# Performance work log

Hardware: AMD Instinct MI355X
Metric: run time of the kernel (lower is better)

Reference implementation:

```python
import jax, jax.numpy as jnp
import numpy as np

N = 63001
F_IN = 512
F_OUT = 256
E = 2_000_000
LRELU_ALPHA = 0.2


def setup_inputs() -> dict:
    key = jax.random.key(0)
    ks = jax.random.split(key, 10)
    x = jax.random.normal(ks[0], (N, F_IN), dtype=jnp.float32)
    values = jax.random.uniform(ks[1], (E,), dtype=jnp.float32)
    edge_index = jax.random.randint(ks[2], (2, E), 0, N, dtype=jnp.int32)
    # learned params: conv1d kernel_size=1 == dense matmuls
    W = jax.random.normal(ks[3], (F_IN, F_OUT), dtype=jnp.float32) * (1.0 / np.sqrt(F_IN))
    a1 = jax.random.normal(ks[4], (F_OUT,), dtype=jnp.float32) * (1.0 / np.sqrt(F_OUT))
    b1 = jnp.zeros((), dtype=jnp.float32)
    a2 = jax.random.normal(ks[5], (F_OUT,), dtype=jnp.float32) * (1.0 / np.sqrt(F_OUT))
    b2 = jnp.zeros((), dtype=jnp.float32)
    b_out = jnp.zeros((F_OUT,), dtype=jnp.float32)
    return {"x": x, "values": values, "edge_index": edge_index,
            "W": W, "a1": a1, "b1": b1, "a2": a2, "b2": b2, "b_out": b_out}


def reference(x, values, edge_index, W, a1, b1, a2, b2, b_out):
    src = edge_index[0]  # row index i of sparse adjacency entry
    dst = edge_index[1]  # col index j

    # conv1d(kernel=1) projections == matmuls
    seq_fts = x @ W                      # [N, F_out]
    f1 = seq_fts @ a1 + b1               # [N]
    f2 = seq_fts @ a2 + b2               # [N]

    # edgewise logits: s_ij * f1_i + s_ij * f2_j  (sparse_add of two masked broadcasts)
    logits = values * (f1[src] + f2[dst])           # [E]
    logits = jax.nn.leaky_relu(logits, LRELU_ALPHA)

    # sparse row-wise softmax over edges grouped by src
    m = jax.ops.segment_max(logits, src, num_segments=N)   # [N]
    p = jnp.exp(logits - m[src])                            # [E]
    denom = jax.ops.segment_sum(p, src, num_segments=N)     # [N]
    coefs = p / denom[src]                                  # [E]

    # SPMM: out_i = sum_j coef_ij * seq_fts_j
    out = jnp.zeros((N, F_OUT), dtype=seq_fts.dtype)
    out = out.at[src].add(coefs[:, None] * seq_fts[dst])

    out = out + b_out                                       # bias_add
    return jax.nn.elu(out)
```

## Files before the change

kernel.cpp:

```cpp
#include <hip/hip_runtime.h>
#include <cstdint>
#include <cstddef>

#define FIN 512
#define FOUT 256
#define LRELU 0.2f
#define NBKT 8
#define BSH 13

typedef __attribute__((ext_vector_type(8))) short bf16x8;
typedef __attribute__((ext_vector_type(8))) unsigned short u16x8;
typedef __attribute__((ext_vector_type(4))) float f32x4;
typedef _Float16 h16x2 __attribute__((ext_vector_type(2)));

#define PERM_LO 0x05040100u
#define PERM_HI 0x07060302u
#define ONE2H   0x3C003C00u

__device__ inline ushort f2bf(float f) {
    union { float f; uint32_t u; } c; c.f = f;
    uint32_t u = c.u;
    return (ushort)((u + 0x7FFF + ((u >> 16) & 1)) >> 16);
}
__device__ inline ushort f2h(float f) {
    union { _Float16 h; ushort u; } c; c.h = (_Float16)f;
    return c.u;
}
__device__ inline h16x2 u2h2(uint32_t u) {
    union { uint32_t u; h16x2 h; } c; c.u = u;
    return c.h;
}

__global__ void prep_wt(const float* __restrict__ W, ushort* __restrict__ WT)
{
    const int idx = blockIdx.x * blockDim.x + threadIdx.x;
    if (idx < FIN * FOUT) {
        const int k = idx >> 8, n = idx & 255;
        WT[(size_t)n * FIN + k] = f2bf(W[(size_t)k * FOUT + n]);
    }
}

#define BM 128
#define BK 64
__global__ __launch_bounds__(512) void gemm_bf16(
    const float* __restrict__ A,
    const ushort* __restrict__ BT,
    ushort* __restrict__ Ch,
    const float* __restrict__ a1, const float* __restrict__ a2,
    const float* __restrict__ b1, const float* __restrict__ b2,
    float* __restrict__ f1, float* __restrict__ f2,
    int M)
{
    __shared__ ushort As[BM * BK];
    __shared__ ushort Bs[FOUT * BK];
    __shared__ float f1s[BM][2];
    __shared__ float f2s[BM][2];
    const int t = threadIdx.x;
    const int lane = t & 63, w = t >> 6;
    const int wm = w & 3, wn = w >> 2;
    const int brow = blockIdx.x * BM;

    f32x4 acc[2][8] = {};

    const int ar = t >> 2;
    const int ak = (t & 3) << 4;
    const int bcol = t >> 1;
    const int bkc = (t & 1) * 4;

    for (int k0 = 0; k0 < FIN; k0 += BK) {
        {
            f32x4 v0, v1, v2, v3;
            const int grow = brow + ar;
            if (grow < M) {
                const f32x4* p = (const f32x4*)(A + (size_t)grow * FIN + k0 + ak);
                v0 = __builtin_nontemporal_load(p + 0);
                v1 = __builtin_nontemporal_load(p + 1);
                v2 = __builtin_nontemporal_load(p + 2);
                v3 = __builtin_nontemporal_load(p + 3);
            } else {
                v0 = v1 = v2 = v3 = (f32x4)0.f;
            }
            u16x8 w0, w1;
            w0[0]=f2bf(v0[0]); w0[1]=f2bf(v0[1]); w0[2]=f2bf(v0[2]); w0[3]=f2bf(v0[3]);
            w0[4]=f2bf(v1[0]); w0[5]=f2bf(v1[1]); w0[6]=f2bf(v1[2]); w0[7]=f2bf(v1[3]);
            w1[0]=f2bf(v2[0]); w1[1]=f2bf(v2[1]); w1[2]=f2bf(v2[2]); w1[3]=f2bf(v2[3]);
            w1[4]=f2bf(v3[0]); w1[5]=f2bf(v3[1]); w1[6]=f2bf(v3[2]); w1[7]=f2bf(v3[3]);
            const int c0 = ((ak >> 3) + 0) ^ (ar & 7);
            const int c1 = ((ak >> 3) + 1) ^ (ar & 7);
            *(u16x8*)(&As[ar * BK + (c0 << 3)]) = w0;
            *(u16x8*)(&As[ar * BK + (c1 << 3)]) = w1;
        }
        {
            const ushort* bp = BT + (size_t)bcol * FIN + k0;
#pragma unroll
            for (int j = 0; j < 4; ++j) {
                const int c = bkc + j;
                u16x8 bv = *(const u16x8*)(bp + (c << 3));
                *(u16x8*)(&Bs[bcol * BK + ((c ^ (bcol & 7)) << 3)]) = bv;
            }
        }
        __syncthreads();

#pragma unroll
        for (int kk = 0; kk < 2; ++kk) {
            const int kc = kk * 4 + (lane >> 4);
            bf16x8 af[2], bfr[8];
#pragma unroll
            for (int m = 0; m < 2; ++m) {
                const int row = wm * 32 + m * 16 + (lane & 15);
                af[m] = *(const bf16x8*)(&As[row * BK + ((kc ^ (row & 7)) << 3)]);
            }
#pragma unroll
            for (int n = 0; n < 8; ++n) {
                const int col = wn * 128 + n * 16 + (lane & 15);
                bfr[n] = *(const bf16x8*)(&Bs[col * BK + ((kc ^ (col & 7)) << 3)]);
            }
#pragma unroll
            for (int m = 0; m < 2; ++m)
#pragma unroll
                for (int n = 0; n < 8; ++n)
                    acc[m][n] = __builtin_amdgcn_mfma_f32_16x16x32_bf16(
                        af[m], bfr[n], acc[m][n], 0, 0, 0);
        }
        __syncthreads();
    }

    float a1c[8], a2c[8];
#pragma unroll
    for (int n = 0; n < 8; ++n) {
        const int col = wn * 128 + n * 16 + (lane & 15);
        a1c[n] = a1[col];
        a2c[n] = a2[col];
    }
    const int cbase = wn * 128 + (lane & 15);
#pragma unroll
    for (int m = 0; m < 2; ++m) {
#pragma unroll
        for (int reg = 0; reg < 4; ++reg) {
            const int rloc = wm * 32 + m * 16 + (lane >> 4) * 4 + reg;
            const int r = brow + rloc;
            float p1 = 0.f, p2 = 0.f;
#pragma unroll
            for (int n = 0; n < 8; ++n) {
                p1 += acc[m][n][reg] * a1c[n];
                p2 += acc[m][n][reg] * a2c[n];
            }
#pragma unroll
            for (int off = 1; off < 16; off <<= 1) {
                p1 += __shfl_xor(p1, off);
                p2 += __shfl_xor(p2, off);
            }
            if ((lane & 15) == 0) {
                f1s[rloc][wn] = p1;
                f2s[rloc][wn] = p2;
            }
            if (r < M) {
#pragma unroll
                for (int n = 0; n < 8; ++n)
                    Ch[(size_t)r * FOUT + cbase + n * 16] = f2h(acc[m][n][reg]);
            }
        }
    }
    __syncthreads();
    if (t < BM) {
        const int r = brow + t;
        if (r < M) {
            f1[r] = f1s[t][0] + f1s[t][1] + b1[0];
            f2[r] = f2s[t][0] + f2s[t][1] + b2[0];
        }
    }
}

__global__ void pos_kernel(const int* __restrict__ src, const int* __restrict__ dst,
                           int* __restrict__ cnt, int* __restrict__ pos, int E)
{
    int i = (blockIdx.x * blockDim.x + threadIdx.x) * 4;
    if (i + 4 <= E) {
        const int4 s = *(const int4*)(src + i);
        const int4 d = *(const int4*)(dst + i);
        int4 p;
        p.x = atomicAdd(&cnt[s.x * NBKT + (d.x >> BSH)], 1);
        p.y = atomicAdd(&cnt[s.y * NBKT + (d.y >> BSH)], 1);
        p.z = atomicAdd(&cnt[s.z * NBKT + (d.z >> BSH)], 1);
        p.w = atomicAdd(&cnt[s.w * NBKT + (d.w >> BSH)], 1);
        *(int4*)(pos + i) = p;
    } else {
        for (; i < E; ++i) pos[i] = atomicAdd(&cnt[src[i] * NBKT + (dst[i] >> BSH)], 1);
    }
}

__global__ __launch_bounds__(1024) void scan_blk(const int* __restrict__ cnt,
                                                 int* __restrict__ btot, int K)
{
    __shared__ int s[1024];
    const int t = threadIdx.x;
    const int idx = blockIdx.x * 1024 + t;
    s[t] = (idx < K) ? cnt[idx] : 0;
    __syncthreads();
    for (int off = 512; off; off >>= 1) {
        if (t < off) s[t] += s[t + off];
        __syncthreads();
    }
    if (t == 0) btot[blockIdx.x] = s[0];
}

__global__ __launch_bounds__(1024) void scan_top(const int* __restrict__ btot,
                                                 int* __restrict__ boff, int nb)
{
    __shared__ int s[1024];
    const int t = threadIdx.x;
    const int mine = (t < nb) ? btot[t] : 0;
    s[t] = mine;
    __syncthreads();
    for (int off = 1; off < 1024; off <<= 1) {
        const int u = (t >= off) ? s[t - off] : 0;
        __syncthreads();
        s[t] += u;
        __syncthreads();
    }
    if (t < nb) boff[t] = s[t] - mine;
}

__global__ __launch_bounds__(1024) void scan_out(const int* __restrict__ cnt,
                                                 const int* __restrict__ boff,
                                                 int* __restrict__ koff, int K)
{
    __shared__ int s[1024];
    const int t = threadIdx.x;
    const int b = blockIdx.x;
    const int idx = b * 1024 + t;
    const int v = (idx < K) ? cnt[idx] : 0;
    s[t] = v;
    __syncthreads();
    for (int off = 1; off < 1024; off <<= 1) {
        const int u = (t >= off) ? s[t - off] : 0;
        __syncthreads();
        s[t] += u;
        __syncthreads();
    }
    if (idx < K)      koff[idx] = boff[b] + s[t] - v;
    if (idx == K - 1) koff[K]   = boff[b] + s[t];
}

__global__ void scatter_p(const int* __restrict__ src, const int* __restrict__ dst,
                          const float* __restrict__ values, const int* __restrict__ pos,
                          const float* __restrict__ f1, const float* __restrict__ f2,
                          const int* __restrict__ koff,
                          unsigned long long* __restrict__ pd, int E)
{
    const int i = blockIdx.x * blockDim.x + threadIdx.x;
    if (i < E) {
        const int s = src[i];
        const int d = dst[i];
        float lg = values[i] * (f1[s] + f2[d]);
        lg = (lg > 0.f) ? lg : LRELU * lg;
        const float p = __expf(lg);
        const unsigned long long rec = (unsigned long long)f2h(p) |
                                       ((unsigned long long)(uint32_t)d << 32);
        __builtin_nontemporal_store(rec, &pd[koff[s * NBKT + (d >> BSH)] + pos[i]]);
    }
}

__global__ __launch_bounds__(256) void spmm_kernel(
    const ushort* __restrict__ seq,
    const unsigned long long* __restrict__ pd,
    const int* __restrict__ koff, const float* __restrict__ b_out,
    float* __restrict__ out, int N)
{
    const int w = threadIdx.x >> 6, lane = threadIdx.x & 63;
    const int row = blockIdx.x * 4 + w;
    if (row >= N) return;
    const int start = __builtin_amdgcn_readfirstlane(koff[row * NBKT]);
    const int end   = __builtin_amdgcn_readfirstlane(koff[(row + 1) * NBKT]);

    const ushort* seql = seq + lane * 4;
    float acc0 = 0.f, acc1 = 0.f, acc2 = 0.f, acc3 = 0.f, den = 0.f;
    const h16x2 one2 = u2h2(ONE2H);

    int t = start;
    for (; t + 4 <= end; t += 4) {
        const unsigned long long q0 = pd[t],     q1 = pd[t + 1];
        const unsigned long long q2 = pd[t + 2], q3 = pd[t + 3];
        const int d0 = (int)(q0 >> 32), d1 = (int)(q1 >> 32);
        const int d2 = (int)(q2 >> 32), d3 = (int)(q3 >> 32);
        const uint2 s0 = *(const uint2*)(seql + (size_t)d0 * FOUT);
        const uint2 s1 = *(const uint2*)(seql + (size_t)d1 * FOUT);
        const uint2 s2 = *(const uint2*)(seql + (size_t)d2 * FOUT);
        const uint2 s3 = *(const uint2*)(seql + (size_t)d3 * FOUT);
        const h16x2 ppA = u2h2(((uint32_t)q0 & 0xffffu) | ((uint32_t)q1 << 16));
        const h16x2 ppB = u2h2(((uint32_t)q2 & 0xffffu) | ((uint32_t)q3 << 16));
        acc0 = __builtin_amdgcn_fdot2(ppA, u2h2(__builtin_amdgcn_perm(s1.x, s0.x, PERM_LO)), acc0, false);
        acc1 = __builtin_amdgcn_fdot2(ppA, u2h2(__builtin_amdgcn_perm(s1.x, s0.x, PERM_HI)), acc1, false);
        acc2 = __builtin_amdgcn_fdot2(ppA, u2h2(__builtin_amdgcn_perm(s1.y, s0.y, PERM_LO)), acc2, false);
        acc3 = __builtin_amdgcn_fdot2(ppA, u2h2(__builtin_amdgcn_perm(s1.y, s0.y, PERM_HI)), acc3, false);
        den  = __builtin_amdgcn_fdot2(ppA, one2, den, false);
        acc0 = __builtin_amdgcn_fdot2(ppB, u2h2(__builtin_amdgcn_perm(s3.x, s2.x, PERM_LO)), acc0, false);
        acc1 = __builtin_amdgcn_fdot2(ppB, u2h2(__builtin_amdgcn_perm(s3.x, s2.x, PERM_HI)), acc1, false);
        acc2 = __builtin_amdgcn_fdot2(ppB, u2h2(__builtin_amdgcn_perm(s3.y, s2.y, PERM_LO)), acc2, false);
        acc3 = __builtin_amdgcn_fdot2(ppB, u2h2(__builtin_amdgcn_perm(s3.y, s2.y, PERM_HI)), acc3, false);
        den  = __builtin_amdgcn_fdot2(ppB, one2, den, false);
    }
    if (t + 2 <= end) {
        const unsigned long long q0 = pd[t], q1 = pd[t + 1];
        const int d0 = (int)(q0 >> 32), d1 = (int)(q1 >> 32);
        const uint2 s0 = *(const uint2*)(seql + (size_t)d0 * FOUT);
        const uint2 s1 = *(const uint2*)(seql + (size_t)d1 * FOUT);
        const h16x2 ppA = u2h2(((uint32_t)q0 & 0xffffu) | ((uint32_t)q1 << 16));
        acc0 = __builtin_amdgcn_fdot2(ppA, u2h2(__builtin_amdgcn_perm(s1.x, s0.x, PERM_LO)), acc0, false);
        acc1 = __builtin_amdgcn_fdot2(ppA, u2h2(__builtin_amdgcn_perm(s1.x, s0.x, PERM_HI)), acc1, false);
        acc2 = __builtin_amdgcn_fdot2(ppA, u2h2(__builtin_amdgcn_perm(s1.y, s0.y, PERM_LO)), acc2, false);
        acc3 = __builtin_amdgcn_fdot2(ppA, u2h2(__builtin_amdgcn_perm(s1.y, s0.y, PERM_HI)), acc3, false);
        den  = __builtin_amdgcn_fdot2(ppA, one2, den, false);
        t += 2;
    }
    if (t < end) {
        const unsigned long long q0 = pd[t];
        const int d0 = (int)(q0 >> 32);
        const uint2 s0 = *(const uint2*)(seql + (size_t)d0 * FOUT);
        const h16x2 ppA = u2h2((uint32_t)q0 & 0xffffu);
        acc0 = __builtin_amdgcn_fdot2(ppA, u2h2(__builtin_amdgcn_perm(s0.x, s0.x, PERM_LO)), acc0, false);
        acc1 = __builtin_amdgcn_fdot2(ppA, u2h2(__builtin_amdgcn_perm(s0.x, s0.x, PERM_HI)), acc1, false);
        acc2 = __builtin_amdgcn_fdot2(ppA, u2h2(__builtin_amdgcn_perm(s0.y, s0.y, PERM_LO)), acc2, false);
        acc3 = __builtin_amdgcn_fdot2(ppA, u2h2(__builtin_amdgcn_perm(s0.y, s0.y, PERM_HI)), acc3, false);
        den  = __builtin_amdgcn_fdot2(ppA, one2, den, false);
    }

    const float inv = (end > start) ? 1.f / den : 0.f;
    const float4 bo = *(const float4*)(b_out + lane * 4);
    f32x4 o;
    o[0] = acc0 * inv + bo.x;
    o[1] = acc1 * inv + bo.y;
    o[2] = acc2 * inv + bo.z;
    o[3] = acc3 * inv + bo.w;
    o[0] = (o[0] > 0.f) ? o[0] : expm1f(o[0]);
    o[1] = (o[1] > 0.f) ? o[1] : expm1f(o[1]);
    o[2] = (o[2] > 0.f) ? o[2] : expm1f(o[2]);
    o[3] = (o[3] > 0.f) ? o[3] : expm1f(o[3]);
    __builtin_nontemporal_store(o, (f32x4*)(out + (size_t)row * FOUT + lane * 4));
}

extern "C" void kernel_launch(void* const* d_in, const int* in_sizes, int n_in,
                              void* d_out, int out_size, void* d_ws, size_t ws_size,
                              hipStream_t stream)
{
    const float* x      = (const float*)d_in[0];
    const float* values = (const float*)d_in[1];
    const int*   ei     = (const int*)d_in[2];
    const float* W      = (const float*)d_in[3];
    const float* a1     = (const float*)d_in[4];
    const float* b1     = (const float*)d_in[5];
    const float* a2     = (const float*)d_in[6];
    const float* b2     = (const float*)d_in[7];
    const float* b_out  = (const float*)d_in[8];
    float* out = (float*)d_out;

    const int N = in_sizes[0] / FIN;
    const int E = in_sizes[1];
    const int* src = ei;
    const int* dst = ei + E;
    const int K = N * NBKT;

    auto alignup = [](size_t v) { return (v + 255) & ~(size_t)255; };
    char* ws = (char*)d_ws;
    size_t off = 0;
    ushort* seqh  = (ushort*)(ws + off); off = alignup(off + (size_t)N * FOUT * 2);
    ushort* WT    = (ushort*)(ws + off); off = alignup(off + (size_t)FIN * FOUT * 2);
    float*  f1    = (float*)(ws + off);  off = alignup(off + (size_t)N * 4);
    float*  f2    = (float*)(ws + off);  off = alignup(off + (size_t)N * 4);
    int*    cnt   = (int*)(ws + off);    off = alignup(off + (size_t)K * 4);
    int*    koff  = (int*)(ws + off);    off = alignup(off + (size_t)(K + 1) * 4);
    int*    btot  = (int*)(ws + off);    off = alignup(off + (size_t)1024 * 4);
    int*    boff  = (int*)(ws + off);    off = alignup(off + (size_t)1024 * 4);
    int*    pos   = (int*)(ws + off);    off = alignup(off + (size_t)E * 4);
    unsigned long long* pd = (unsigned long long*)(ws + off); off = alignup(off + (size_t)E * 8);
    (void)ws_size;

    const int nbk = (K + 1023) / 1024;

    hipMemsetAsync(cnt, 0, (size_t)K * 4, stream);

    pos_kernel<<<(E / 4 + 255) / 256, 256, 0, stream>>>(src, dst, cnt, pos, E);
    scan_blk<<<nbk, 1024, 0, stream>>>(cnt, btot, K);
    scan_top<<<1, 1024, 0, stream>>>(btot, boff, nbk);
    scan_out<<<nbk, 1024, 0, stream>>>(cnt, boff, koff, K);

    prep_wt<<<(FIN * FOUT + 255) / 256, 256, 0, stream>>>(W, WT);
    gemm_bf16<<<(N + BM - 1) / BM, 512, 0, stream>>>(x, WT, seqh, a1, a2, b1, b2,
                                                     f1, f2, N);

    scatter_p<<<(E + 255) / 256, 256, 0, stream>>>(src, dst, values, pos, f1, f2,
                                                   koff, pd, E);

    spmm_kernel<<<(N + 3) / 4, 256, 0, stream>>>(seqh, pd, koff, b_out, out, N);
}
```

Baseline: 357.5 us.

## Pack edge records to 32 bits, use cursor atomics, and DMA GEMM B tiles into LDS

```diff
diff --git a/kernel.cpp b/kernel.cpp
--- a/kernel.cpp
+++ b/kernel.cpp
@@ -1,4 +1,5 @@
 #include <hip/hip_runtime.h>
+#include <hip/hip_bf16.h>
 #include <cstdint>
 #include <cstddef>
 
@@ -18,9 +19,9 @@
 #define ONE2H   0x3C003C00u
 
 __device__ inline ushort f2bf(float f) {
-    union { float f; uint32_t u; } c; c.f = f;
-    uint32_t u = c.u;
-    return (ushort)((u + 0x7FFF + ((u >> 16) & 1)) >> 16);
+    __hip_bfloat16 h = __float2bfloat16(f);
+    union { __hip_bfloat16 h; ushort u; } c; c.h = h;
+    return c.u;
 }
 __device__ inline ushort f2h(float f) {
     union { _Float16 h; ushort u; } c; c.h = (_Float16)f;
@@ -29,6 +30,9 @@
 __device__ inline h16x2 u2h2(uint32_t u) {
     union { uint32_t u; h16x2 h; } c; c.u = u;
     return c.h;
+}
+__device__ inline float hdot2(h16x2 pp, uint32_t sv, float acc) {
+    return __builtin_amdgcn_fdot2(pp, u2h2(sv), acc, false);
 }
 
 __global__ void prep_wt(const float* __restrict__ W, ushort* __restrict__ WT)
@@ -64,10 +68,22 @@
 
     const int ar = t >> 2;
     const int ak = (t & 3) << 4;
-    const int bcol = t >> 1;
-    const int bkc = (t & 1) * 4;
+
+    const int bcol8 = (lane >> 3);
+    const int bslot = lane & 7;
+    const int bcdat = bslot ^ (bcol8 & 7);
 
     for (int k0 = 0; k0 < FIN; k0 += BK) {
+#pragma unroll
+        for (int j = 0; j < 4; ++j) {
+            const int grp = w * 4 + j;
+            const int col = grp * 8 + bcol8;
+            const ushort* gsrc = BT + (size_t)col * FIN + k0 + bcdat * 8;
+            ushort* ldst = &Bs[grp * 512];
+            __builtin_amdgcn_global_load_lds(
+                (const __attribute__((address_space(1))) void*)gsrc,
+                (__attribute__((address_space(3))) void*)ldst, 16, 0, 0);
+        }
         {
             f32x4 v0, v1, v2, v3;
             const int grow = brow + ar;
@@ -90,15 +106,6 @@
             *(u16x8*)(&As[ar * BK + (c0 << 3)]) = w0;
             *(u16x8*)(&As[ar * BK + (c1 << 3)]) = w1;
         }
-        {
-            const ushort* bp = BT + (size_t)bcol * FIN + k0;
-#pragma unroll
-            for (int j = 0; j < 4; ++j) {
-                const int c = bkc + j;
-                u16x8 bv = *(const u16x8*)(bp + (c << 3));
-                *(u16x8*)(&Bs[bcol * BK + ((c ^ (bcol & 7)) << 3)]) = bv;
-            }
-        }
         __syncthreads();
 
 #pragma unroll
@@ -171,21 +178,19 @@
     }
 }
 
-__global__ void pos_kernel(const int* __restrict__ src, const int* __restrict__ dst,
-                           int* __restrict__ cnt, int* __restrict__ pos, int E)
+__global__ void cnt_kernel(const int* __restrict__ src, const int* __restrict__ dst,
+                           int* __restrict__ cnt, int E)
 {
     int i = (blockIdx.x * blockDim.x + threadIdx.x) * 4;
     if (i + 4 <= E) {
         const int4 s = *(const int4*)(src + i);
         const int4 d = *(const int4*)(dst + i);
-        int4 p;
-        p.x = atomicAdd(&cnt[s.x * NBKT + (d.x >> BSH)], 1);
-        p.y = atomicAdd(&cnt[s.y * NBKT + (d.y >> BSH)], 1);
-        p.z = atomicAdd(&cnt[s.z * NBKT + (d.z >> BSH)], 1);
-        p.w = atomicAdd(&cnt[s.w * NBKT + (d.w >> BSH)], 1);
-        *(int4*)(pos + i) = p;
+        atomicAdd(&cnt[s.x * NBKT + (d.x >> BSH)], 1);
+        atomicAdd(&cnt[s.y * NBKT + (d.y >> BSH)], 1);
+        atomicAdd(&cnt[s.z * NBKT + (d.z >> BSH)], 1);
+        atomicAdd(&cnt[s.w * NBKT + (d.w >> BSH)], 1);
     } else {
-        for (; i < E; ++i) pos[i] = atomicAdd(&cnt[src[i] * NBKT + (dst[i] >> BSH)], 1);
+        for (; i < E; ++i) atomicAdd(&cnt[src[i] * NBKT + (dst[i] >> BSH)], 1);
     }
 }
 
@@ -223,7 +228,8 @@
 
 __global__ __launch_bounds__(1024) void scan_out(const int* __restrict__ cnt,
                                                  const int* __restrict__ boff,
-                                                 int* __restrict__ koff, int K)
+                                                 int* __restrict__ koff,
+                                                 int* __restrict__ cursor, int K)
 {
     __shared__ int s[1024];
     const int t = threadIdx.x;
@@ -238,15 +244,19 @@
         s[t] += u;
         __syncthreads();
     }
-    if (idx < K)      koff[idx] = boff[b] + s[t] - v;
-    if (idx == K - 1) koff[K]   = boff[b] + s[t];
+    if (idx < K) {
+        const int e = boff[b] + s[t] - v;
+        koff[idx] = e;
+        cursor[idx] = e;
+    }
+    if (idx == K - 1) koff[K] = boff[b] + s[t];
 }
 
 __global__ void scatter_p(const int* __restrict__ src, const int* __restrict__ dst,
-                          const float* __restrict__ values, const int* __restrict__ pos,
+                          const float* __restrict__ values,
                           const float* __restrict__ f1, const float* __restrict__ f2,
-                          const int* __restrict__ koff,
-                          unsigned long long* __restrict__ pd, int E)
+                          int* __restrict__ cursor,
+                          uint32_t* __restrict__ pd, int E)
 {
     const int i = blockIdx.x * blockDim.x + threadIdx.x;
     if (i < E) {
@@ -255,15 +265,14 @@
         float lg = values[i] * (f1[s] + f2[d]);
         lg = (lg > 0.f) ? lg : LRELU * lg;
         const float p = __expf(lg);
-        const unsigned long long rec = (unsigned long long)f2h(p) |
-                                       ((unsigned long long)(uint32_t)d << 32);
-        __builtin_nontemporal_store(rec, &pd[koff[s * NBKT + (d >> BSH)] + pos[i]]);
+        const int slot = atomicAdd(&cursor[s * NBKT + (d >> BSH)], 1);
+        pd[slot] = ((uint32_t)d << 16) | (uint32_t)f2h(p);
     }
 }
 
 __global__ __launch_bounds__(256) void spmm_kernel(
     const ushort* __restrict__ seq,
-    const unsigned long long* __restrict__ pd,
+    const uint32_t* __restrict__ pd,
     const int* __restrict__ koff, const float* __restrict__ b_out,
     float* __restrict__ out, int N)
 {
@@ -278,51 +287,44 @@
     const h16x2 one2 = u2h2(ONE2H);
 
     int t = start;
-    for (; t + 4 <= end; t += 4) {
-        const unsigned long long q0 = pd[t],     q1 = pd[t + 1];
-        const unsigned long long q2 = pd[t + 2], q3 = pd[t + 3];
-        const int d0 = (int)(q0 >> 32), d1 = (int)(q1 >> 32);
-        const int d2 = (int)(q2 >> 32), d3 = (int)(q3 >> 32);
-        const uint2 s0 = *(const uint2*)(seql + (size_t)d0 * FOUT);
-        const uint2 s1 = *(const uint2*)(seql + (size_t)d1 * FOUT);
-        const uint2 s2 = *(const uint2*)(seql + (size_t)d2 * FOUT);
-        const uint2 s3 = *(const uint2*)(seql + (size_t)d3 * FOUT);
-        const h16x2 ppA = u2h2(((uint32_t)q0 & 0xffffu) | ((uint32_t)q1 << 16));
-        const h16x2 ppB = u2h2(((uint32_t)q2 & 0xffffu) | ((uint32_t)q3 << 16));
-        acc0 = __builtin_amdgcn_fdot2(ppA, u2h2(__builtin_amdgcn_perm(s1.x, s0.x, PERM_LO)), acc0, false);
-        acc1 = __builtin_amdgcn_fdot2(ppA, u2h2(__builtin_amdgcn_perm(s1.x, s0.x, PERM_HI)), acc1, false);
-        acc2 = __builtin_amdgcn_fdot2(ppA, u2h2(__builtin_amdgcn_perm(s1.y, s0.y, PERM_LO)), acc2, false);
-        acc3 = __builtin_amdgcn_fdot2(ppA, u2h2(__builtin_amdgcn_perm(s1.y, s0.y, PERM_HI)), acc3, false);
-        den  = __builtin_amdgcn_fdot2(ppA, one2, den, false);
-        acc0 = __builtin_amdgcn_fdot2(ppB, u2h2(__builtin_amdgcn_perm(s3.x, s2.x, PERM_LO)), acc0, false);
-        acc1 = __builtin_amdgcn_fdot2(ppB, u2h2(__builtin_amdgcn_perm(s3.x, s2.x, PERM_HI)), acc1, false);
-        acc2 = __builtin_amdgcn_fdot2(ppB, u2h2(__builtin_amdgcn_perm(s3.y, s2.y, PERM_LO)), acc2, false);
-        acc3 = __builtin_amdgcn_fdot2(ppB, u2h2(__builtin_amdgcn_perm(s3.y, s2.y, PERM_HI)), acc3, false);
-        den  = __builtin_amdgcn_fdot2(ppB, one2, den, false);
-    }
-    if (t + 2 <= end) {
-        const unsigned long long q0 = pd[t], q1 = pd[t + 1];
-        const int d0 = (int)(q0 >> 32), d1 = (int)(q1 >> 32);
-        const uint2 s0 = *(const uint2*)(seql + (size_t)d0 * FOUT);
-        const uint2 s1 = *(const uint2*)(seql + (size_t)d1 * FOUT);
-        const h16x2 ppA = u2h2(((uint32_t)q0 & 0xffffu) | ((uint32_t)q1 << 16));
-        acc0 = __builtin_amdgcn_fdot2(ppA, u2h2(__builtin_amdgcn_perm(s1.x, s0.x, PERM_LO)), acc0, false);
-        acc1 = __builtin_amdgcn_fdot2(ppA, u2h2(__builtin_amdgcn_perm(s1.x, s0.x, PERM_HI)), acc1, false);
-        acc2 = __builtin_amdgcn_fdot2(ppA, u2h2(__builtin_amdgcn_perm(s1.y, s0.y, PERM_LO)), acc2, false);
-        acc3 = __builtin_amdgcn_fdot2(ppA, u2h2(__builtin_amdgcn_perm(s1.y, s0.y, PERM_HI)), acc3, false);
-        den  = __builtin_amdgcn_fdot2(ppA, one2, den, false);
-        t += 2;
+    for (; t + 8 <= end; t += 8) {
+        uint32_t q[8];
+#pragma unroll
+        for (int j = 0; j < 8; ++j) q[j] = pd[t + j];
+        uint2 s[8];
+#pragma unroll
+        for (int j = 0; j < 8; ++j)
+            s[j] = *(const uint2*)(seql + (size_t)(q[j] >> 16) * FOUT);
+#pragma unroll
+        for (int j = 0; j < 8; j += 2) {
+            const h16x2 pp = u2h2((q[j] & 0xffffu) | (q[j + 1] << 16));
+            acc0 = hdot2(pp, __builtin_amdgcn_perm(s[j+1].x, s[j].x, PERM_LO), acc0);
+            acc1 = hdot2(pp, __builtin_amdgcn_perm(s[j+1].x, s[j].x, PERM_HI), acc1);
+            acc2 = hdot2(pp, __builtin_amdgcn_perm(s[j+1].y, s[j].y, PERM_LO), acc2);
+            acc3 = hdot2(pp, __builtin_amdgcn_perm(s[j+1].y, s[j].y, PERM_HI), acc3);
+            den  = hdot2(pp, ONE2H, den);
+        }
+    }
+    for (; t + 2 <= end; t += 2) {
+        const uint32_t q0 = pd[t], q1 = pd[t + 1];
+        const uint2 s0 = *(const uint2*)(seql + (size_t)(q0 >> 16) * FOUT);
+        const uint2 s1 = *(const uint2*)(seql + (size_t)(q1 >> 16) * FOUT);
+        const h16x2 pp = u2h2((q0 & 0xffffu) | (q1 << 16));
+        acc0 = hdot2(pp, __builtin_amdgcn_perm(s1.x, s0.x, PERM_LO), acc0);
+        acc1 = hdot2(pp, __builtin_amdgcn_perm(s1.x, s0.x, PERM_HI), acc1);
+        acc2 = hdot2(pp, __builtin_amdgcn_perm(s1.y, s0.y, PERM_LO), acc2);
+        acc3 = hdot2(pp, __builtin_amdgcn_perm(s1.y, s0.y, PERM_HI), acc3);
+        den  = hdot2(pp, ONE2H, den);
     }
     if (t < end) {
-        const unsigned long long q0 = pd[t];
-        const int d0 = (int)(q0 >> 32);
-        const uint2 s0 = *(const uint2*)(seql + (size_t)d0 * FOUT);
-        const h16x2 ppA = u2h2((uint32_t)q0 & 0xffffu);
-        acc0 = __builtin_amdgcn_fdot2(ppA, u2h2(__builtin_amdgcn_perm(s0.x, s0.x, PERM_LO)), acc0, false);
-        acc1 = __builtin_amdgcn_fdot2(ppA, u2h2(__builtin_amdgcn_perm(s0.x, s0.x, PERM_HI)), acc1, false);
-        acc2 = __builtin_amdgcn_fdot2(ppA, u2h2(__builtin_amdgcn_perm(s0.y, s0.y, PERM_LO)), acc2, false);
-        acc3 = __builtin_amdgcn_fdot2(ppA, u2h2(__builtin_amdgcn_perm(s0.y, s0.y, PERM_HI)), acc3, false);
-        den  = __builtin_amdgcn_fdot2(ppA, one2, den, false);
+        const uint32_t q0 = pd[t];
+        const uint2 s0 = *(const uint2*)(seql + (size_t)(q0 >> 16) * FOUT);
+        const h16x2 pp = u2h2(q0 & 0xffffu);
+        acc0 = hdot2(pp, __builtin_amdgcn_perm(s0.x, s0.x, PERM_LO), acc0);
+        acc1 = hdot2(pp, __builtin_amdgcn_perm(s0.x, s0.x, PERM_HI), acc1);
+        acc2 = hdot2(pp, __builtin_amdgcn_perm(s0.y, s0.y, PERM_LO), acc2);
+        acc3 = hdot2(pp, __builtin_amdgcn_perm(s0.y, s0.y, PERM_HI), acc3);
+        den  = hdot2(pp, ONE2H, den);
     }
 
     const float inv = (end > start) ? 1.f / den : 0.f;
@@ -363,33 +365,33 @@
     auto alignup = [](size_t v) { return (v + 255) & ~(size_t)255; };
     char* ws = (char*)d_ws;
     size_t off = 0;
-    ushort* seqh  = (ushort*)(ws + off); off = alignup(off + (size_t)N * FOUT * 2);
-    ushort* WT    = (ushort*)(ws + off); off = alignup(off + (size_t)FIN * FOUT * 2);
-    float*  f1    = (float*)(ws + off);  off = alignup(off + (size_t)N * 4);
-    float*  f2    = (float*)(ws + off);  off = alignup(off + (size_t)N * 4);
-    int*    cnt   = (int*)(ws + off);    off = alignup(off + (size_t)K * 4);
-    int*    koff  = (int*)(ws + off);    off = alignup(off + (size_t)(K + 1) * 4);
-    int*    btot  = (int*)(ws + off);    off = alignup(off + (size_t)1024 * 4);
-    int*    boff  = (int*)(ws + off);    off = alignup(off + (size_t)1024 * 4);
-    int*    pos   = (int*)(ws + off);    off = alignup(off + (size_t)E * 4);
-    unsigned long long* pd = (unsigned long long*)(ws + off); off = alignup(off + (size_t)E * 8);
+    ushort*   seqh   = (ushort*)(ws + off);   off = alignup(off + (size_t)N * FOUT * 2);
+    ushort*   WT     = (ushort*)(ws + off);   off = alignup(off + (size_t)FIN * FOUT * 2);
+    float*    f1     = (float*)(ws + off);    off = alignup(off + (size_t)N * 4);
+    float*    f2     = (float*)(ws + off);    off = alignup(off + (size_t)N * 4);
+    int*      cnt    = (int*)(ws + off);      off = alignup(off + (size_t)K * 4);
+    int*      koff   = (int*)(ws + off);      off = alignup(off + (size_t)(K + 1) * 4);
+    int*      cursor = (int*)(ws + off);      off = alignup(off + (size_t)K * 4);
+    int*      btot   = (int*)(ws + off);      off = alignup(off + (size_t)1024 * 4);
+    int*      boff   = (int*)(ws + off);      off = alignup(off + (size_t)1024 * 4);
+    uint32_t* pd     = (uint32_t*)(ws + off); off = alignup(off + (size_t)E * 4);
     (void)ws_size;
 
     const int nbk = (K + 1023) / 1024;
 
     hipMemsetAsync(cnt, 0, (size_t)K * 4, stream);
 
-    pos_kernel<<<(E / 4 + 255) / 256, 256, 0, stream>>>(src, dst, cnt, pos, E);
+    cnt_kernel<<<(E / 4 + 255) / 256, 256, 0, stream>>>(src, dst, cnt, E);
     scan_blk<<<nbk, 1024, 0, stream>>>(cnt, btot, K);
     scan_top<<<1, 1024, 0, stream>>>(btot, boff, nbk);
-    scan_out<<<nbk, 1024, 0, stream>>>(cnt, boff, koff, K);
+    scan_out<<<nbk, 1024, 0, stream>>>(cnt, boff, koff, cursor, K);
 
     prep_wt<<<(FIN * FOUT + 255) / 256, 256, 0, stream>>>(W, WT);
     gemm_bf16<<<(N + BM - 1) / BM, 512, 0, stream>>>(x, WT, seqh, a1, a2, b1, b2,
                                                      f1, f2, N);
 
-    scatter_p<<<(E + 255) / 256, 256, 0, stream>>>(src, dst, values, pos, f1, f2,
-                                                   koff, pd, E);
+    scatter_p<<<(E + 255) / 256, 256, 0, stream>>>(src, dst, values, f1, f2,
+                                                   cursor, pd, E);
 
     spmm_kernel<<<(N + 3) / 4, 256, 0, stream>>>(seqh, pd, koff, b_out, out, N);
 }
```

New measurement: 389.0 us. 1.09x slower.
